# Performance work log

Hardware: AMD Instinct MI355X
Metric: run time of the kernel (lower is better)

The kernel has to match this reference:

```python
import jax, jax.numpy as jnp
import numpy as np

B, S, C, L = 4, 32, 256, 512
H = 8
D = L // H  # head_size = 64
EPS = 1e-5


def _layernorm(x, g, b):
    mu = jnp.mean(x, axis=-1, keepdims=True)
    var = jnp.var(x, axis=-1, keepdims=True)
    return (x - mu) * jax.lax.rsqrt(var + EPS) * g + b


def setup_inputs() -> dict:
    key = jax.random.key(0)
    ks = jax.random.split(key, 12)
    s = 1.0 / np.sqrt(L)
    return {
        "x": jax.random.normal(ks[0], (B, S, C, L), dtype=jnp.float32),
        # per-head QKV weights, stacked: [H, D, L] (torch Linear(L, D, bias=False).weight)
        "Wq": jax.random.normal(ks[1], (H, D, L), dtype=jnp.float32) * s,
        "Wk": jax.random.normal(ks[2], (H, D, L), dtype=jnp.float32) * s,
        "Wv": jax.random.normal(ks[3], (H, D, L), dtype=jnp.float32) * s,
        # output projection Linear(L, L)
        "Wo": jax.random.normal(ks[4], (L, L), dtype=jnp.float32) * s,
        "bo": jnp.zeros((L,), dtype=jnp.float32),
        # FFN Linear(L, 4L) -> ReLU -> Linear(4L, L)
        "W1": jax.random.normal(ks[5], (4 * L, L), dtype=jnp.float32) * s,
        "b1": jnp.zeros((4 * L,), dtype=jnp.float32),
        "W2": jax.random.normal(ks[6], (L, 4 * L), dtype=jnp.float32) * (1.0 / np.sqrt(4 * L)),
        "b2": jnp.zeros((L,), dtype=jnp.float32),
        # LayerNorm params
        "g1": jnp.ones((L,), dtype=jnp.float32),
        "be1": jnp.zeros((L,), dtype=jnp.float32),
        "g2": jnp.ones((L,), dtype=jnp.float32),
        "be2": jnp.zeros((L,), dtype=jnp.float32),
    }


def reference(x, Wq, Wk, Wv, Wo, bo, W1, b1, W2, b2, g1, be1, g2, be2):
    # --- regional multi-head self-attention (pre-LN, residual) ---
    h = _layernorm(x, g1, be1)                        # [B,S,C,L]
    q = jnp.einsum('bscl,hdl->bhscd', h, Wq)          # [B,H,S,C,D]
    k = jnp.einsum('bscl,hdl->bhscd', h, Wk)
    v = jnp.einsum('bscl,hdl->bhscd', h, Wv)
    wei = jnp.einsum('bhsqd,bhskd->bhsqk', q, k) * (D ** -0.5)  # [B,H,S,C,C]
    wei = jax.nn.softmax(wei, axis=-1)                # no causal mask (tril unused)
    out = jnp.einsum('bhsqk,bhskd->bhsqd', wei, v)    # [B,H,S,C,D]
    out = jnp.transpose(out, (0, 2, 3, 1, 4)).reshape(x.shape[0], x.shape[1], x.shape[2], H * D)
    out = out @ Wo.T + bo                             # proj Linear(L, L)
    x = x + out
    # --- feed-forward (pre-LN, residual) ---
    h2 = _layernorm(x, g2, be2)
    ff = jax.nn.relu(h2 @ W1.T + b1) @ W2.T + b2      # [B,S,C,L]
    return x + ff
```

## Files before the change

### kernel.cpp

```cpp
#include <hip/hip_runtime.h>
#include <cstdint>
#include <cstddef>

#define NTOK 32768
#define LDIM 512
#define HN 8
#define HD 64
#define CC 256
#define FFD 2048

typedef __bf16 bf16x8 __attribute__((ext_vector_type(8)));
typedef float f32x4 __attribute__((ext_vector_type(4)));
typedef unsigned short u16;
typedef unsigned int u32;

__device__ __forceinline__ u16 f2bf(float f) {
  u32 u = __float_as_uint(f);
  u32 r = (u + 0x7fffu + ((u >> 16) & 1u)) >> 16;
  return (u16)r;
}

__device__ __forceinline__ void gload_lds16(const void* g, void* l) {
  __builtin_amdgcn_global_load_lds(
      (__attribute__((address_space(1))) void*)(void*)g,
      (__attribute__((address_space(3))) void*)l, 16, 0, 0);
}

__global__ void k_convall(const float* __restrict__ Wq, const float* __restrict__ Wk,
                          const float* __restrict__ Wv, const float* __restrict__ Wo,
                          const float* __restrict__ W1, const float* __restrict__ W2,
                          u16* __restrict__ wqkv, u16* __restrict__ wo,
                          u16* __restrict__ w1, u16* __restrict__ w2) {
  const int NW = 262144;
  const int MW = 1048576;
  const int TOT = 4 * NW + 2 * MW;
  int i = blockIdx.x * blockDim.x + threadIdx.x;
  const int st = gridDim.x * blockDim.x;
  for (; i < TOT; i += st) {
    if (i < NW) wqkv[i] = f2bf(Wq[i]);
    else if (i < 2 * NW) wqkv[i] = f2bf(Wk[i - NW]);
    else if (i < 3 * NW) wqkv[i] = f2bf(Wv[i - 2 * NW]);
    else if (i < 4 * NW) wo[i - 3 * NW] = f2bf(Wo[i - 3 * NW]);
    else if (i < 4 * NW + MW) w1[i - 4 * NW] = f2bf(W1[i - 4 * NW]);
    else w2[i - 4 * NW - MW] = f2bf(W2[i - 4 * NW - MW]);
  }
}

__global__ __launch_bounds__(256) void k_ln(const float* __restrict__ x,
                                            const float* __restrict__ gam,
                                            const float* __restrict__ bet,
                                            u16* __restrict__ out) {
  const int row = blockIdx.x * 4 + (threadIdx.x >> 6);
  const int lane = threadIdx.x & 63;
  const float4* xr = (const float4*)(x + (size_t)row * LDIM);
  float4 a = xr[lane * 2], b = xr[lane * 2 + 1];
  float s = a.x + a.y + a.z + a.w + b.x + b.y + b.z + b.w;
  float q = a.x * a.x + a.y * a.y + a.z * a.z + a.w * a.w +
            b.x * b.x + b.y * b.y + b.z * b.z + b.w * b.w;
#pragma unroll
  for (int m = 1; m < 64; m <<= 1) { s += __shfl_xor(s, m); q += __shfl_xor(q, m); }
  const float mean = s * (1.f / LDIM);
  const float rs = rsqrtf(q * (1.f / LDIM) - mean * mean + 1e-5f);
  const int c0 = lane * 8;
  const float4* g4 = (const float4*)(gam + c0);
  const float4* b4 = (const float4*)(bet + c0);
  float4 ga = g4[0], gb = g4[1], ba = b4[0], bb = b4[1];
  float vin[8] = {a.x, a.y, a.z, a.w, b.x, b.y, b.z, b.w};
  float vg[8]  = {ga.x, ga.y, ga.z, ga.w, gb.x, gb.y, gb.z, gb.w};
  float vb[8]  = {ba.x, ba.y, ba.z, ba.w, bb.x, bb.y, bb.z, bb.w};
  u16 o[8];
#pragma unroll
  for (int i = 0; i < 8; ++i) o[i] = f2bf((vin[i] - mean) * rs * vg[i] + vb[i]);
  *(bf16x8*)(out + (size_t)row * LDIM + c0) = *(bf16x8*)o;
}


__device__ __forceinline__ void stage_half128(const u16* __restrict__ g, int K,
                                              u16* __restrict__ lds, int t) {
#pragma unroll
  for (int i = 0; i < 2; ++i) {
    const int p = i * 512 + t;
    const int r = p >> 3;
    const int c = ((p & 7) ^ (r & 7)) << 3;
    gload_lds16(g + (size_t)r * K + c, lds + ((i * 512 + (t & ~63)) << 3));
  }
}

__device__ __forceinline__ bf16x8 ldsfrag64(const u16* __restrict__ s, int R, int ck) {
  return *(const bf16x8*)(s + R * 64 + ((ck ^ (R & 7)) << 3));
}

#define VM0 asm volatile("s_waitcnt vmcnt(0)" ::: "memory")
#define LGKM0 asm volatile("s_waitcnt lgkmcnt(0)" ::: "memory")
#define BARRIER asm volatile("s_barrier" ::: "memory")

template <int EPI>
__global__ __launch_bounds__(512, 2) void k_gemm8(const u16* __restrict__ A,
                                                  const u16* __restrict__ Bw, int K,
                                                  const float* __restrict__ bias,
                                                  const float* __restrict__ resid,
                                                  void* __restrict__ outp, int ldc,
                                                  int bmN) {
  extern __shared__ u16 lds_g[];
  const int t = threadIdx.x;
  const int lane = t & 63;
  const int w = t >> 6;
  const int wm = w >> 2, wn = w & 3;
  const int rl = lane & 15;
  const int kq = lane >> 4;
  const int nwg = gridDim.x;
  const int cpx = nwg >> 3;
  const int id = blockIdx.x;
  const int sid = (id & 7) * cpx + (id >> 3);
  const int bm = sid % bmN, bn = sid / bmN;

  const u16* Ag = A + (size_t)bm * 256 * K;
  const u16* Bg = Bw + (size_t)bn * 256 * K;
  u16* const SAm = lds_g + (wm ? 16384 : 0);
  u16* const SBm = lds_g + 32768 + ((wn >> 1) ? 16384 : 0);
  const int rBl = (wn & 1) * 64;

  f32x4 acc[8][4] = {};

  stage_half128(Ag, K, lds_g + 0, t);
  stage_half128(Ag + (size_t)128 * K, K, lds_g + 16384, t);
  stage_half128(Bg, K, lds_g + 32768, t);
  stage_half128(Bg + (size_t)128 * K, K, lds_g + 49152, t);
  VM0;
  BARRIER;

  const int NT = K >> 6;
  for (int T = 0; T < NT; ++T) {
    const int par = T & 1, nx = par ^ 1;
    const bool hn = (T + 1 < NT);
    const u16* An = Ag + (size_t)(T + 1) * 64;
    const u16* Bn = Bg + (size_t)(T + 1) * 64;
    bf16x8 b[4][2];
#pragma unroll
    for (int p = 0; p < 4; ++p) {
      bf16x8 a[2][2];
#pragma unroll
      for (int rf = 0; rf < 2; ++rf)
#pragma unroll
        for (int kk = 0; kk < 2; ++kk)
          a[rf][kk] = ldsfrag64(SAm + par * 8192, p * 32 + rf * 16 + rl, kk * 4 + kq);
      if (p == 0) {
#pragma unroll
        for (int n = 0; n < 4; ++n)
#pragma unroll
          for (int kk = 0; kk < 2; ++kk)
            b[n][kk] = ldsfrag64(SBm + par * 8192, rBl + n * 16 + rl, kk * 4 + kq);
        if (hn) {
          stage_half128(An, K, lds_g + nx * 8192, t);
          stage_half128(Bn, K, lds_g + 32768 + nx * 8192, t);
        }
      } else if (p == 1) {
        if (hn) {
          stage_half128(An + (size_t)128 * K, K, lds_g + 16384 + nx * 8192, t);
          stage_half128(Bn + (size_t)128 * K, K, lds_g + 49152 + nx * 8192, t);
        }
      }
      BARRIER;
      LGKM0;
      __builtin_amdgcn_sched_barrier(0);
      __builtin_amdgcn_s_setprio(1);
#pragma unroll
      for (int rf = 0; rf < 2; ++rf)
#pragma unroll
        for (int n = 0; n < 4; ++n) {
          acc[p * 2 + rf][n] =
              __builtin_amdgcn_mfma_f32_16x16x32_bf16(a[rf][0], b[n][0], acc[p * 2 + rf][n], 0, 0, 0);
          acc[p * 2 + rf][n] =
              __builtin_amdgcn_mfma_f32_16x16x32_bf16(a[rf][1], b[n][1], acc[p * 2 + rf][n], 0, 0, 0);
        }
      __builtin_amdgcn_s_setprio(0);
      if (p == 3) VM0;
      BARRIER;
    }
  }

  const int rg = (lane >> 4) * 4;
  const int cl = lane & 15;
#pragma unroll
  for (int mi = 0; mi < 8; ++mi)
#pragma unroll
    for (int n = 0; n < 4; ++n) {
      const int mg = bm * 256 + wm * 128 + mi * 16 + rg;
      const int og = bn * 256 + wn * 64 + n * 16 + cl;
#pragma unroll
      for (int r = 0; r < 4; ++r) {
        float v = acc[mi][n][r];
        size_t idx = (size_t)(mg + r) * ldc + og;
        if (EPI == 0) {
          ((u16*)outp)[idx] = f2bf(v);
        } else if (EPI == 1) {
          ((float*)outp)[idx] = resid[idx] + v + bias[og];
        } else if (EPI == 2) {
          ((u16*)outp)[idx] = f2bf(fmaxf(v + bias[og], 0.f));
        } else {
          ((float*)outp)[idx] = ((float*)outp)[idx] + v + bias[og];
        }
      }
    }
}

__device__ __forceinline__ int swz(int row, int col) {
  return row * 64 + (col ^ ((row & 7) << 3));
}

__global__ __launch_bounds__(256) void k_attn(const u16* __restrict__ qkv,
                                              u16* __restrict__ attn) {
  __shared__ u16 Ks[64 * 64];
  __shared__ u16 Vt[64 * 64];
  __shared__ u16 Pl[4 * 64 * 64];
  const int t = threadIdx.x, lane = t & 63, w = t >> 6;
  const int region = blockIdx.x >> 3;
  const int h = blockIdx.x & 7;
  const size_t n0 = (size_t)region * CC;
  const int qb = w * 64;
  const int rl = lane & 15;
  const int kg = (lane >> 4) * 8;
  u16* Pw = Pl + w * 4096;

  bf16x8 aq[4][2];
#pragma unroll
  for (int f = 0; f < 4; ++f)
#pragma unroll
    for (int ks = 0; ks < 2; ++ks)
      aq[f][ks] = *(const bf16x8*)&qkv[(n0 + qb + f * 16 + rl) * 1536 + h * 64 + ks * 32 + kg];

  f32x4 oacc[4][4] = {};
  float mrun[4][4], lrun[4][4];
#pragma unroll
  for (int i = 0; i < 4; ++i)
#pragma unroll
    for (int j = 0; j < 4; ++j) { mrun[i][j] = -1e30f; lrun[i][j] = 0.f; }

  const int sr = t >> 2;
  const int sc = (t & 3) * 16;
  for (int kt = 0; kt < 4; ++kt) {
    if (kt) __syncthreads();
    {
      const u16* kp = &qkv[(n0 + kt * 64 + sr) * 1536 + 512 + h * 64 + sc];
      bf16x8 k0 = *(const bf16x8*)kp;
      bf16x8 k1 = *(const bf16x8*)(kp + 8);
      *(bf16x8*)&Ks[swz(sr, sc)] = k0;
      *(bf16x8*)&Ks[swz(sr, sc + 8)] = k1;
      const u16* vp = &qkv[(n0 + kt * 64 + sr) * 1536 + 1024 + h * 64 + sc];
      bf16x8 v0 = *(const bf16x8*)vp;
      bf16x8 v1 = *(const bf16x8*)(vp + 8);
#pragma unroll
      for (int i = 0; i < 8; ++i) Vt[swz(sc + i, sr)] = ((u16*)&v0)[i];
#pragma unroll
      for (int i = 0; i < 8; ++i) Vt[swz(sc + 8 + i, sr)] = ((u16*)&v1)[i];
    }
    __syncthreads();
    f32x4 sacc[4][4] = {};
#pragma unroll
    for (int ks = 0; ks < 2; ++ks) {
      bf16x8 bk[4];
#pragma unroll
      for (int f = 0; f < 4; ++f) bk[f] = *(const bf16x8*)&Ks[swz(f * 16 + rl, ks * 32 + kg)];
#pragma unroll
      for (int i = 0; i < 4; ++i)
#pragma unroll
        for (int j = 0; j < 4; ++j)
          sacc[i][j] = __builtin_amdgcn_mfma_f32_16x16x32_bf16(aq[i][ks], bk[j], sacc[i][j], 0, 0, 0);
    }
#pragma unroll
    for (int i = 0; i < 4; ++i)
#pragma unroll
      for (int j = 0; j < 4; ++j)
#pragma unroll
        for (int r = 0; r < 4; ++r) sacc[i][j][r] *= 0.125f;
#pragma unroll
    for (int i = 0; i < 4; ++i) {
#pragma unroll
      for (int r = 0; r < 4; ++r) {
        float v = fmaxf(fmaxf(sacc[i][0][r], sacc[i][1][r]), fmaxf(sacc[i][2][r], sacc[i][3][r]));
#pragma unroll
        for (int m = 1; m < 16; m <<= 1) v = fmaxf(v, __shfl_xor(v, m));
        float mnew = fmaxf(mrun[i][r], v);
        float fac = __expf(mrun[i][r] - mnew);
        mrun[i][r] = mnew;
        float ps = 0.f;
#pragma unroll
        for (int fn = 0; fn < 4; ++fn) {
          float p = __expf(sacc[i][fn][r] - mnew);
          sacc[i][fn][r] = p;
          ps += p;
        }
#pragma unroll
        for (int m = 1; m < 16; m <<= 1) ps += __shfl_xor(ps, m);
        lrun[i][r] = lrun[i][r] * fac + ps;
#pragma unroll
        for (int fd = 0; fd < 4; ++fd) oacc[i][fd][r] *= fac;
      }
#pragma unroll
      for (int fn = 0; fn < 4; ++fn)
#pragma unroll
        for (int r = 0; r < 4; ++r)
          Pw[swz(i * 16 + (lane >> 4) * 4 + r, fn * 16 + rl)] = f2bf(sacc[i][fn][r]);
    }
#pragma unroll
    for (int ks = 0; ks < 2; ++ks) {
      bf16x8 ap[4], bv[4];
#pragma unroll
      for (int f = 0; f < 4; ++f) ap[f] = *(const bf16x8*)&Pw[swz(f * 16 + rl, ks * 32 + kg)];
#pragma unroll
      for (int f = 0; f < 4; ++f) bv[f] = *(const bf16x8*)&Vt[swz(f * 16 + rl, ks * 32 + kg)];
#pragma unroll
      for (int i = 0; i < 4; ++i)
#pragma unroll
        for (int j = 0; j < 4; ++j)
          oacc[i][j] = __builtin_amdgcn_mfma_f32_16x16x32_bf16(ap[i], bv[j], oacc[i][j], 0, 0, 0);
    }
  }
#pragma unroll
  for (int i = 0; i < 4; ++i)
#pragma unroll
    for (int fd = 0; fd < 4; ++fd)
#pragma unroll
      for (int r = 0; r < 4; ++r) {
        float v = oacc[i][fd][r] / lrun[i][r];
        attn[(n0 + qb + i * 16 + (lane >> 4) * 4 + r) * 512 + h * 64 + fd * 16 + rl] = f2bf(v);
      }
}

extern "C" void kernel_launch(void* const* d_in, const int* in_sizes, int n_in,
                              void* d_out, int out_size, void* d_ws, size_t ws_size,
                              hipStream_t stream) {
  (void)in_sizes; (void)n_in; (void)out_size; (void)ws_size;
  const float* x   = (const float*)d_in[0];
  const float* Wq  = (const float*)d_in[1];
  const float* Wk  = (const float*)d_in[2];
  const float* Wv  = (const float*)d_in[3];
  const float* Wo  = (const float*)d_in[4];
  const float* bo  = (const float*)d_in[5];
  const float* W1  = (const float*)d_in[6];
  const float* b1  = (const float*)d_in[7];
  const float* W2  = (const float*)d_in[8];
  const float* b2  = (const float*)d_in[9];
  const float* g1  = (const float*)d_in[10];
  const float* be1 = (const float*)d_in[11];
  const float* g2  = (const float*)d_in[12];
  const float* be2 = (const float*)d_in[13];
  float* out = (float*)d_out;

  char* ws = (char*)d_ws;
  u16* wqkv = (u16*)(ws + 0);
  u16* wo   = (u16*)(ws + 1572864);
  u16* w1   = (u16*)(ws + 2097152);
  u16* w2   = (u16*)(ws + 4194304);
  u16* regA = (u16*)(ws + 6291456);
  u16* regB = (u16*)(ws + 39845888);

  const size_t LDSB = 131072;

  k_convall<<<1024, 256, 0, stream>>>(Wq, Wk, Wv, Wo, W1, W2, wqkv, wo, w1, w2);
  k_ln<<<NTOK / 4, 256, 0, stream>>>(x, g1, be1, regA);
  k_gemm8<0><<<dim3(128 * 6), 512, LDSB, stream>>>(regA, wqkv, 512, nullptr, nullptr, regB, 1536, 128);
  k_attn<<<dim3(4 * 32 * 8), 256, 0, stream>>>(regB, regA);
  k_gemm8<1><<<dim3(128 * 2), 512, LDSB, stream>>>(regA, wo, 512, bo, x, out, 512, 128);
  k_ln<<<NTOK / 4, 256, 0, stream>>>(out, g2, be2, regA);
  k_gemm8<2><<<dim3(128 * 8), 512, LDSB, stream>>>(regA, w1, 512, b1, nullptr, regB, 2048, 128);
  k_gemm8<3><<<dim3(128 * 2), 512, LDSB, stream>>>(regB, w2, 2048, b2, nullptr, out, 512, 128);
}
```

Before: 448.1 us.

## Software-pipeline LDS A-fragment loads and drop per-phase barriers in GEMM loop

Restructures the GEMM K-loop so the B fragments and the first A fragments load up front, and the next phase's A fragments are prefetched into registers while the current MFMAs run. The per-phase s_barrier, lgkmcnt wait, sched_barrier and setprio calls are removed, leaving one vmcnt wait and one barrier per K tile. The aim is to cut synchronisation stalls and overlap LDS reads with matrix math. The cost is higher register pressure from the extra fragments, and scheduling is left entirely to the compiler.

```diff
diff --git a/kernel.cpp b/kernel.cpp
--- a/kernel.cpp
+++ b/kernel.cpp
@@ -91,7 +91,6 @@
 }
 
 #define VM0 asm volatile("s_waitcnt vmcnt(0)" ::: "memory")
-#define LGKM0 asm volatile("s_waitcnt lgkmcnt(0)" ::: "memory")
 #define BARRIER asm volatile("s_barrier" ::: "memory")
 
 template <int EPI>
@@ -135,35 +134,37 @@
     const bool hn = (T + 1 < NT);
     const u16* An = Ag + (size_t)(T + 1) * 64;
     const u16* Bn = Bg + (size_t)(T + 1) * 64;
-    bf16x8 b[4][2];
+    const u16* sA = SAm + par * 8192;
+    const u16* sB = SBm + par * 8192;
+
+    bf16x8 b[4][2], a[2][2], an[2][2];
+#pragma unroll
+    for (int n = 0; n < 4; ++n)
+#pragma unroll
+      for (int kk = 0; kk < 2; ++kk)
+        b[n][kk] = ldsfrag64(sB, rBl + n * 16 + rl, kk * 4 + kq);
+#pragma unroll
+    for (int rf = 0; rf < 2; ++rf)
+#pragma unroll
+      for (int kk = 0; kk < 2; ++kk)
+        a[rf][kk] = ldsfrag64(sA, rf * 16 + rl, kk * 4 + kq);
+
 #pragma unroll
     for (int p = 0; p < 4; ++p) {
-      bf16x8 a[2][2];
-#pragma unroll
-      for (int rf = 0; rf < 2; ++rf)
-#pragma unroll
-        for (int kk = 0; kk < 2; ++kk)
-          a[rf][kk] = ldsfrag64(SAm + par * 8192, p * 32 + rf * 16 + rl, kk * 4 + kq);
-      if (p == 0) {
-#pragma unroll
-        for (int n = 0; n < 4; ++n)
+      if (p < 3) {
+#pragma unroll
+        for (int rf = 0; rf < 2; ++rf)
 #pragma unroll
           for (int kk = 0; kk < 2; ++kk)
-            b[n][kk] = ldsfrag64(SBm + par * 8192, rBl + n * 16 + rl, kk * 4 + kq);
-        if (hn) {
-          stage_half128(An, K, lds_g + nx * 8192, t);
-          stage_half128(Bn, K, lds_g + 32768 + nx * 8192, t);
-        }
-      } else if (p == 1) {
-        if (hn) {
-          stage_half128(An + (size_t)128 * K, K, lds_g + 16384 + nx * 8192, t);
-          stage_half128(Bn + (size_t)128 * K, K, lds_g + 49152 + nx * 8192, t);
-        }
-      }
-      BARRIER;
-      LGKM0;
-      __builtin_amdgcn_sched_barrier(0);
-      __builtin_amdgcn_s_setprio(1);
+            an[rf][kk] = ldsfrag64(sA, (p + 1) * 32 + rf * 16 + rl, kk * 4 + kq);
+      }
+      if (p == 0 && hn) {
+        stage_half128(An, K, lds_g + nx * 8192, t);
+        stage_half128(Bn, K, lds_g + 32768 + nx * 8192, t);
+      } else if (p == 1 && hn) {
+        stage_half128(An + (size_t)128 * K, K, lds_g + 16384 + nx * 8192, t);
+        stage_half128(Bn + (size_t)128 * K, K, lds_g + 49152 + nx * 8192, t);
+      }
 #pragma unroll
       for (int rf = 0; rf < 2; ++rf)
 #pragma unroll
@@ -173,10 +174,14 @@
           acc[p * 2 + rf][n] =
               __builtin_amdgcn_mfma_f32_16x16x32_bf16(a[rf][1], b[n][1], acc[p * 2 + rf][n], 0, 0, 0);
         }
-      __builtin_amdgcn_s_setprio(0);
-      if (p == 3) VM0;
-      BARRIER;
-    }
+#pragma unroll
+      for (int rf = 0; rf < 2; ++rf)
+#pragma unroll
+        for (int kk = 0; kk < 2; ++kk)
+          a[rf][kk] = an[rf][kk];
+    }
+    VM0;
+    BARRIER;
   }
 
   const int rg = (lane >> 4) * 4;
```

Measured after the change: 462.1 us. 3.1% more time.

## Replace 256x256 8-wave GEMM with simpler 128x128 4-wave double-buffered GEMM

Applied to the files above, without the earlier changes.

Replaces the 256x256-tile, 512-thread GEMM kernel with a 128x128-tile, 256-thread kernel. Each k-step stages the next 64-wide K slice of A and B together, then does one fragment load and MFMA pass per wave, with one wait and barrier per iteration. The hand-tuned phase interleaving, setprio and split-barrier scheduling are dropped. This quadruples the workgroup count and halves LDS per block to improve occupancy and tail balance, but lowers operand reuse per tile and raises global and L2 traffic for every GEMM.

```diff
diff --git a/kernel.cpp b/kernel.cpp
--- a/kernel.cpp
+++ b/kernel.cpp
@@ -75,14 +75,18 @@
 }
 
 
-__device__ __forceinline__ void stage_half128(const u16* __restrict__ g, int K,
-                                              u16* __restrict__ lds, int t) {
-#pragma unroll
-  for (int i = 0; i < 2; ++i) {
-    const int p = i * 512 + t;
+__device__ __forceinline__ void stage_tile128(const u16* __restrict__ Ag,
+                                              const u16* __restrict__ Bg, int K, int k0,
+                                              u16* __restrict__ SA, u16* __restrict__ SB,
+                                              int t) {
+#pragma unroll
+  for (int i = 0; i < 4; ++i) {
+    const int p = i * 256 + t;
     const int r = p >> 3;
     const int c = ((p & 7) ^ (r & 7)) << 3;
-    gload_lds16(g + (size_t)r * K + c, lds + ((i * 512 + (t & ~63)) << 3));
+    const int dst = (i * 256 + (t & ~63)) << 3;
+    gload_lds16(Ag + (size_t)r * K + k0 + c, SA + dst);
+    gload_lds16(Bg + (size_t)r * K + k0 + c, SB + dst);
   }
 }
 
@@ -91,21 +95,20 @@
 }
 
 #define VM0 asm volatile("s_waitcnt vmcnt(0)" ::: "memory")
-#define LGKM0 asm volatile("s_waitcnt lgkmcnt(0)" ::: "memory")
 #define BARRIER asm volatile("s_barrier" ::: "memory")
 
 template <int EPI>
-__global__ __launch_bounds__(512, 2) void k_gemm8(const u16* __restrict__ A,
-                                                  const u16* __restrict__ Bw, int K,
-                                                  const float* __restrict__ bias,
-                                                  const float* __restrict__ resid,
-                                                  void* __restrict__ outp, int ldc,
-                                                  int bmN) {
+__global__ __launch_bounds__(256, 2) void k_gemm128(const u16* __restrict__ A,
+                                                    const u16* __restrict__ Bw, int K,
+                                                    const float* __restrict__ bias,
+                                                    const float* __restrict__ resid,
+                                                    void* __restrict__ outp, int ldc,
+                                                    int bmN) {
   extern __shared__ u16 lds_g[];
   const int t = threadIdx.x;
   const int lane = t & 63;
   const int w = t >> 6;
-  const int wm = w >> 2, wn = w & 3;
+  const int wm = w >> 1, wn = w & 1;
   const int rl = lane & 15;
   const int kq = lane >> 4;
   const int nwg = gridDim.x;
@@ -114,79 +117,50 @@
   const int sid = (id & 7) * cpx + (id >> 3);
   const int bm = sid % bmN, bn = sid / bmN;
 
-  const u16* Ag = A + (size_t)bm * 256 * K;
-  const u16* Bg = Bw + (size_t)bn * 256 * K;
-  u16* const SAm = lds_g + (wm ? 16384 : 0);
-  u16* const SBm = lds_g + 32768 + ((wn >> 1) ? 16384 : 0);
-  const int rBl = (wn & 1) * 64;
-
-  f32x4 acc[8][4] = {};
-
-  stage_half128(Ag, K, lds_g + 0, t);
-  stage_half128(Ag + (size_t)128 * K, K, lds_g + 16384, t);
-  stage_half128(Bg, K, lds_g + 32768, t);
-  stage_half128(Bg + (size_t)128 * K, K, lds_g + 49152, t);
+  const u16* Ag = A + (size_t)bm * 128 * K;
+  const u16* Bg = Bw + (size_t)bn * 128 * K;
+
+  f32x4 acc[4][4] = {};
+
+  stage_tile128(Ag, Bg, K, 0, lds_g, lds_g + 16384, t);
   VM0;
   BARRIER;
 
   const int NT = K >> 6;
   for (int T = 0; T < NT; ++T) {
     const int par = T & 1, nx = par ^ 1;
-    const bool hn = (T + 1 < NT);
-    const u16* An = Ag + (size_t)(T + 1) * 64;
-    const u16* Bn = Bg + (size_t)(T + 1) * 64;
-    bf16x8 b[4][2];
-#pragma unroll
-    for (int p = 0; p < 4; ++p) {
-      bf16x8 a[2][2];
-#pragma unroll
-      for (int rf = 0; rf < 2; ++rf)
-#pragma unroll
-        for (int kk = 0; kk < 2; ++kk)
-          a[rf][kk] = ldsfrag64(SAm + par * 8192, p * 32 + rf * 16 + rl, kk * 4 + kq);
-      if (p == 0) {
-#pragma unroll
-        for (int n = 0; n < 4; ++n)
-#pragma unroll
-          for (int kk = 0; kk < 2; ++kk)
-            b[n][kk] = ldsfrag64(SBm + par * 8192, rBl + n * 16 + rl, kk * 4 + kq);
-        if (hn) {
-          stage_half128(An, K, lds_g + nx * 8192, t);
-          stage_half128(Bn, K, lds_g + 32768 + nx * 8192, t);
-        }
-      } else if (p == 1) {
-        if (hn) {
-          stage_half128(An + (size_t)128 * K, K, lds_g + 16384 + nx * 8192, t);
-          stage_half128(Bn + (size_t)128 * K, K, lds_g + 49152 + nx * 8192, t);
-        }
-      }
-      BARRIER;
-      LGKM0;
-      __builtin_amdgcn_sched_barrier(0);
-      __builtin_amdgcn_s_setprio(1);
-#pragma unroll
-      for (int rf = 0; rf < 2; ++rf)
-#pragma unroll
-        for (int n = 0; n < 4; ++n) {
-          acc[p * 2 + rf][n] =
-              __builtin_amdgcn_mfma_f32_16x16x32_bf16(a[rf][0], b[n][0], acc[p * 2 + rf][n], 0, 0, 0);
-          acc[p * 2 + rf][n] =
-              __builtin_amdgcn_mfma_f32_16x16x32_bf16(a[rf][1], b[n][1], acc[p * 2 + rf][n], 0, 0, 0);
-        }
-      __builtin_amdgcn_s_setprio(0);
-      if (p == 3) VM0;
-      BARRIER;
-    }
+    if (T + 1 < NT)
+      stage_tile128(Ag, Bg, K, (T + 1) << 6, lds_g + nx * 8192,
+                    lds_g + 16384 + nx * 8192, t);
+    const u16* sA = lds_g + par * 8192;
+    const u16* sB = lds_g + 16384 + par * 8192;
+    bf16x8 a[4][2], b[4][2];
+#pragma unroll
+    for (int f = 0; f < 4; ++f)
+#pragma unroll
+      for (int kk = 0; kk < 2; ++kk) {
+        a[f][kk] = ldsfrag64(sA, wm * 64 + f * 16 + rl, kk * 4 + kq);
+        b[f][kk] = ldsfrag64(sB, wn * 64 + f * 16 + rl, kk * 4 + kq);
+      }
+#pragma unroll
+    for (int f = 0; f < 4; ++f)
+#pragma unroll
+      for (int n = 0; n < 4; ++n) {
+        acc[f][n] = __builtin_amdgcn_mfma_f32_16x16x32_bf16(a[f][0], b[n][0], acc[f][n], 0, 0, 0);
+        acc[f][n] = __builtin_amdgcn_mfma_f32_16x16x32_bf16(a[f][1], b[n][1], acc[f][n], 0, 0, 0);
+      }
+    VM0;
+    BARRIER;
   }
 
   const int rg = (lane >> 4) * 4;
   const int cl = lane & 15;
 #pragma unroll
-  for (int mi = 0; mi < 8; ++mi)
+  for (int mi = 0; mi < 4; ++mi)
 #pragma unroll
     for (int n = 0; n < 4; ++n) {
-      const int mg = bm * 256 + wm * 128 + mi * 16 + rg;
-      const int og = bn * 256 + wn * 64 + n * 16 + cl;
+      const int mg = bm * 128 + wm * 64 + mi * 16 + rg;
+      const int og = bn * 128 + wn * 64 + n * 16 + cl;
 #pragma unroll
       for (int r = 0; r < 4; ++r) {
         float v = acc[mi][n][r];
@@ -355,14 +329,14 @@
   u16* regA = (u16*)(ws + 6291456);
   u16* regB = (u16*)(ws + 39845888);
 
-  const size_t LDSB = 131072;
+  const size_t LDSB = 65536;
 
   k_convall<<<1024, 256, 0, stream>>>(Wq, Wk, Wv, Wo, W1, W2, wqkv, wo, w1, w2);
   k_ln<<<NTOK / 4, 256, 0, stream>>>(x, g1, be1, regA);
-  k_gemm8<0><<<dim3(128 * 6), 512, LDSB, stream>>>(regA, wqkv, 512, nullptr, nullptr, regB, 1536, 128);
+  k_gemm128<0><<<dim3(256 * 12), 256, LDSB, stream>>>(regA, wqkv, 512, nullptr, nullptr, regB, 1536, 256);
   k_attn<<<dim3(4 * 32 * 8), 256, 0, stream>>>(regB, regA);
-  k_gemm8<1><<<dim3(128 * 2), 512, LDSB, stream>>>(regA, wo, 512, bo, x, out, 512, 128);
+  k_gemm128<1><<<dim3(256 * 4), 256, LDSB, stream>>>(regA, wo, 512, bo, x, out, 512, 256);
   k_ln<<<NTOK / 4, 256, 0, stream>>>(out, g2, be2, regA);
-  k_gemm8<2><<<dim3(128 * 8), 512, LDSB, stream>>>(regA, w1, 512, b1, nullptr, regB, 2048, 128);
-  k_gemm8<3><<<dim3(128 * 2), 512, LDSB, stream>>>(regB, w2, 2048, b2, nullptr, out, 512, 128);
-}
+  k_gemm128<2><<<dim3(256 * 16), 256, LDSB, stream>>>(regA, w1, 512, b1, nullptr, regB, 2048, 256);
+  k_gemm128<3><<<dim3(256 * 4), 256, LDSB, stream>>>(regB, w2, 2048, b2, nullptr, out, 512, 256);
+}
```

After: 510.6 us. +13.9%, slower.
